# Kernel optimization log

Measured on AMD Instinct MI355X. Metric: run time of the kernel, lower is better.

## Reference

```python
import jax, jax.numpy as jnp
import numpy as np

GROUPS = 32
EPS = 1e-5
NUM_HEADS = 8
HEAD_DIM = 64
CHANNELS = 512


def group_norm(x, scale, bias):
    # x: [b, h, w, c]; normalize over (h, w, channels-within-group)
    b, h, w, c = x.shape
    xg = x.reshape(b, h, w, GROUPS, c // GROUPS)
    mean = jnp.mean(xg, axis=(1, 2, 4), keepdims=True)
    var = jnp.var(xg, axis=(1, 2, 4), keepdims=True)
    xg = (xg - mean) * jax.lax.rsqrt(var + EPS)
    return xg.reshape(b, h, w, c) * scale + bias


def setup_inputs() -> dict:
    key = jax.random.key(0)
    ks = jax.random.split(key, 8)
    b, hs, ws, c = 8, 32, 32, CHANNELS
    inner = NUM_HEADS * HEAD_DIM
    return {
        "x": jax.random.normal(ks[0], (b, hs, ws, c), dtype=jnp.float32),
        "t": jax.random.normal(ks[1], (b,), dtype=jnp.float32),
        "gn_scale": jnp.ones((c,), dtype=jnp.float32),
        "gn_bias": jnp.zeros((c,), dtype=jnp.float32),
        "w_qkv": jax.random.normal(ks[2], (c, 3 * inner), dtype=jnp.float32) * 0.02,
        "b_qkv": jnp.zeros((3 * inner,), dtype=jnp.float32),
        "w_out": jax.random.normal(ks[3], (inner, c), dtype=jnp.float32) * 0.02,
        "b_out": jnp.zeros((c,), dtype=jnp.float32),
    }


def reference(x, t, gn_scale, gn_bias, w_qkv, b_qkv, w_out, b_out):
    b, hs, ws, c = x.shape
    # NOTE: original reassigns x = GroupNorm(x); the residual uses the NORMALIZED x.
    xn = group_norm(x, gn_scale, gn_bias)
    x_flat = xn.reshape(b, hs * ws, c)                      # [b, s, c]
    qkv = x_flat @ w_qkv + b_qkv                            # [b, s, 3*nh*hd]
    qkv = qkv.reshape(b, hs * ws, NUM_HEADS, 3 * HEAD_DIM)
    q, k, v = jnp.split(qkv, 3, axis=-1)                    # each [b, s, nh, hd]
    q = q / jnp.sqrt(jnp.float32(HEAD_DIM))
    q = q.transpose(0, 2, 1, 3)                             # [b, nh, s, hd]
    k = k.transpose(0, 2, 1, 3)
    v = v.transpose(0, 2, 1, 3)
    attn = jax.nn.softmax(jnp.einsum('bhqd,bhkd->bhqk', q, k), axis=-1)
    out = jnp.einsum('bhqk,bhkd->bhqd', attn, v)            # [b, nh, s, hd]
    out = out.transpose(0, 2, 1, 3).reshape(b, hs * ws, NUM_HEADS * HEAD_DIM)
    h = out @ w_out + b_out                                 # [b, s, c]
    h = h.reshape(b, hs, ws, c)
    return xn + h
```

## Files before the change

### kernel.cpp

```cpp
#include <hip/hip_runtime.h>
#include <hip/hip_bf16.h>


#define B_    8
#define S_    1024
#define C_    512
#define NH    8
#define HD    64
#define QKVC  1536
#define GROUPS 32
#define GSIZE  16
#define EPSV   1e-5f
#define QSCL  0.18033688f

using frag8 = __attribute__((ext_vector_type(8))) short;
using f32x4 = __attribute__((ext_vector_type(4))) float;

__device__ __forceinline__ float bf2f(unsigned short u) {
    union { unsigned int i; float f; } v; v.i = ((unsigned int)u) << 16; return v.f;
}
__device__ __forceinline__ unsigned short f2bf(float f) {
    union { float f; unsigned int i; } v; v.f = f;
    unsigned int x = v.i;
    return (unsigned short)((x + 0x7fffu + ((x >> 16) & 1u)) >> 16);
}
__device__ __forceinline__ unsigned int pk2bf(float a, float b) {
    union { float f; unsigned int u; } x, y; x.f = a; y.f = b;
    return __builtin_amdgcn_perm(y.u + 0x8000u, x.u + 0x8000u, 0x07060302u);
}
__device__ __forceinline__ float fexp2(float x) {
#if __has_builtin(__builtin_amdgcn_exp2f)
    return __builtin_amdgcn_exp2f(x);
#else
    return exp2f(x);
#endif
}
__device__ __forceinline__ f32x4 zero4() {
    f32x4 z; z[0] = 0.f; z[1] = 0.f; z[2] = 0.f; z[3] = 0.f; return z;
}
__device__ __forceinline__ void gl_lds(const unsigned short* gp, unsigned short* lp) {
    __builtin_amdgcn_global_load_lds(
        (const __attribute__((address_space(1))) void*)gp,
        (__attribute__((address_space(3))) void*)lp, 16, 0, 0);
}

__global__ __launch_bounds__(256) void prep_kernel(
        const float* __restrict__ w_qkv, const float* __restrict__ w_out,
        unsigned short* __restrict__ wqkvT, unsigned short* __restrict__ woutT,
        const float* __restrict__ x,
        const float* __restrict__ scale, const float* __restrict__ bias,
        unsigned short* __restrict__ xn) {
    __shared__ unsigned short xcache[16384];
    __shared__ float s_red[8];
    int id = blockIdx.x;
    int t = threadIdx.x;
    if (id < 1024) {
        float* tile = (float*)xcache;
        const float* in; unsigned short* out; int N, n0, k0;
        if (id < 768) { in = w_qkv; out = wqkvT; N = QKVC; n0 = (id % 48) * 32; k0 = (id / 48) * 32; }
        else { int i2 = id - 768; in = w_out; out = woutT; N = C_; n0 = (i2 % 16) * 32; k0 = (i2 / 16) * 32; }
        for (int i = 0; i < 4; ++i) {
            int idx = t + i * 256; int r = idx >> 5, c = idx & 31;
            tile[r * 33 + c] = in[(size_t)(k0 + r) * N + n0 + c];
        }
        __syncthreads();
        for (int i = 0; i < 4; ++i) {
            int idx = t + i * 256; int r = idx >> 5, c = idx & 31;
            out[(size_t)(n0 + r) * C_ + k0 + c] = f2bf(tile[c * 33 + r]);
        }
        return;
    }
    int bg = id - 1024;
    int b = bg >> 5, g = bg & 31;
    const float* xb = x + (size_t)b * S_ * C_;

    float sum = 0.f, ss = 0.f;
    for (int i = 0; i < 16; ++i) {
        int idx = t + i * 256;
        int row = idx >> 2, j = idx & 3;
        float4 v = *(const float4*)(xb + (size_t)row * C_ + g * GSIZE + j * 4);
        sum += v.x + v.y + v.z + v.w;
        ss  += v.x * v.x + v.y * v.y + v.z * v.z + v.w * v.w;
        uint2 c;
        c.x = pk2bf(v.x, v.y);
        c.y = pk2bf(v.z, v.w);
        *(uint2*)(&xcache[idx * 4]) = c;
    }
    for (int off = 1; off < 64; off <<= 1) {
        sum += __shfl_xor(sum, off);
        ss  += __shfl_xor(ss,  off);
    }
    int wid = t >> 6;
    if ((t & 63) == 0) { s_red[wid] = sum; s_red[4 + wid] = ss; }
    __syncthreads();
    sum = s_red[0] + s_red[1] + s_red[2] + s_red[3];
    ss  = s_red[4] + s_red[5] + s_red[6] + s_red[7];
    float mean = sum * (1.f / 16384.f);
    float var  = ss * (1.f / 16384.f) - mean * mean;
    float rinv = rsqrtf(var + EPSV);

    float sc[16], bi[16];
    for (int u = 0; u < 16; ++u) {
        sc[u] = scale[g * GSIZE + u];
        bi[u] = bias[g * GSIZE + u];
    }
    for (int i = 0; i < 16; ++i) {
        int idx = t + i * 256;
        int row = idx >> 2, j = idx & 3;
        uint2 c = *(const uint2*)(&xcache[idx * 4]);
        float v0 = bf2f((unsigned short)(c.x & 0xffffu));
        float v1 = bf2f((unsigned short)(c.x >> 16));
        float v2 = bf2f((unsigned short)(c.y & 0xffffu));
        float v3 = bf2f((unsigned short)(c.y >> 16));
        int c0 = j * 4;
        float f0 = (v0 - mean) * rinv * sc[c0 + 0] + bi[c0 + 0];
        float f1 = (v1 - mean) * rinv * sc[c0 + 1] + bi[c0 + 1];
        float f2 = (v2 - mean) * rinv * sc[c0 + 2] + bi[c0 + 2];
        float f3 = (v3 - mean) * rinv * sc[c0 + 3] + bi[c0 + 3];
        uint2 o;
        o.x = pk2bf(f0, f1);
        o.y = pk2bf(f2, f3);
        *(uint2*)(xn + (size_t)b * S_ * C_ + (size_t)row * C_ + g * GSIZE + c0) = o;
    }
}

template<int MODE>
__global__ __launch_bounds__(256) void gemm_kernel(
        const unsigned short* __restrict__ A,
        const unsigned short* __restrict__ Bt,
        const float* __restrict__ bias,
        const unsigned short* __restrict__ resid,
        unsigned short* __restrict__ outA,
        unsigned short* __restrict__ outV,
        float* __restrict__ outF,
        int M, int N, int K) {
    __shared__ unsigned short As[2][128 * 32];
    __shared__ unsigned short Bs[2][128 * 32];
    int m0 = blockIdx.y * 128, n0 = blockIdx.x * 128;
    int t = threadIdx.x;
    int wid = t >> 6, lane = t & 63;
    int quad = lane >> 4, l16 = lane & 15;
    int wm = (wid >> 1) * 64, wn = (wid & 1) * 64;

    f32x4 acc[4][4];
    for (int mi = 0; mi < 4; ++mi)
        for (int ni = 0; ni < 4; ++ni) acc[mi][ni] = zero4();

    int srow = t >> 2, sseg = t & 3;
    auto stage = [&](int k0, int buf) {
        for (int i = 0; i < 2; ++i) {
            gl_lds(A + (size_t)(m0 + i * 64 + srow) * K + k0 + sseg * 8,
                   &As[buf][(size_t)(i * 256 + wid * 64) * 8]);
            gl_lds(Bt + (size_t)(n0 + i * 64 + srow) * K + k0 + sseg * 8,
                   &Bs[buf][(size_t)(i * 256 + wid * 64) * 8]);
        }
    };

    stage(0, 0);
    int nk = K >> 5;
    for (int i = 0; i < nk; ++i) {
        __syncthreads();
        if (i + 1 < nk) stage((i + 1) << 5, (i + 1) & 1);
        int buf = i & 1;

        frag8 bfrag[4], afrag[4];
        for (int ni = 0; ni < 4; ++ni)
            bfrag[ni] = *(const frag8*)(&Bs[buf][(wn + ni * 16 + l16) * 32 + quad * 8]);
        for (int mi = 0; mi < 4; ++mi)
            afrag[mi] = *(const frag8*)(&As[buf][(wm + mi * 16 + l16) * 32 + quad * 8]);

        for (int mi = 0; mi < 4; ++mi)
            for (int ni = 0; ni < 4; ++ni)
                acc[mi][ni] = __builtin_amdgcn_mfma_f32_16x16x32_bf16(
                    afrag[mi], bfrag[ni], acc[mi][ni], 0, 0, 0);
    }

    for (int ni = 0; ni < 4; ++ni) {
        int c0 = n0 + wn + ni * 16;
        float bv = bias[c0 + l16];
        if (MODE == 0) {
            int h = c0 / 192, rr = c0 % 192;
            if (rr >= 128) {
                int d = rr - 128 + l16;
                int bidx = m0 >> 10;
                unsigned short* vp = outV + (((size_t)bidx * NH + h) * HD + d) * S_
                                   + (m0 & 1023) + wm + quad * 4;
                for (int mi = 0; mi < 4; ++mi) {
                    uint2 pk;
                    pk.x = pk2bf(acc[mi][ni][0] + bv, acc[mi][ni][1] + bv);
                    pk.y = pk2bf(acc[mi][ni][2] + bv, acc[mi][ni][3] + bv);
                    *(uint2*)(vp + mi * 16) = pk;
                }
            } else {
                float scl = (rr < 64) ? QSCL : 1.0f;
                int colk = h * 128 + rr + l16;
                for (int mi = 0; mi < 4; ++mi)
                    for (int r = 0; r < 4; ++r) {
                        int row = m0 + wm + mi * 16 + quad * 4 + r;
                        outA[(size_t)row * 1024 + colk] = f2bf((acc[mi][ni][r] + bv) * scl);
                    }
            }
        } else {
            int col = c0 + l16;
            for (int mi = 0; mi < 4; ++mi)
                for (int r = 0; r < 4; ++r) {
                    int row = m0 + wm + mi * 16 + quad * 4 + r;
                    float v = acc[mi][ni][r] + bv + bf2f(resid[(size_t)row * N + col]);
                    outF[(size_t)row * N + col] = v;
                }
        }
    }
}

__global__ __launch_bounds__(256) void attn_kernel(
        const unsigned short* __restrict__ kq,
        const unsigned short* __restrict__ vT,
        unsigned short* __restrict__ attn_out) {
    int i = blockIdx.x;
    int xcd = i & 7, slot = i >> 3;
    int bh = xcd * 8 + (slot >> 4);
    int qt = slot & 15;
    int b = bh >> 3, h = bh & 7;

    int t = threadIdx.x;
    int wid = t >> 6, lane = t & 63, quad = lane >> 4, l16 = lane & 15;
    int q0 = qt * 64 + wid * 16;

    __shared__ unsigned short Ks[2][2][2048];
    __shared__ unsigned short Vs[2][2][2048];

    const unsigned short* qrow = kq + ((size_t)b * S_ + q0 + l16) * 1024 + h * 128;
    frag8 qf0 = *(const frag8*)(qrow + quad * 8);
    frag8 qf1 = *(const frag8*)(qrow + 32 + quad * 8);

    frag8 ones;
    for (int i2 = 0; i2 < 8; ++i2) ones[i2] = (short)0x3f80;

    f32x4 o[4], ol;
    ol = zero4();
    for (int dt = 0; dt < 4; ++dt) o[dt] = zero4();

    const unsigned short* kbase = kq + (size_t)b * S_ * 1024 + h * 128 + 64;
    const unsigned short* vbase = vT + ((size_t)b * NH + h) * HD * S_;

    int kdh = wid & 1, krh = wid >> 1;
    int krow = krh * 16 + (lane >> 2);
    int kseg = lane & 3;
    int vd = wid * 16 + (lane >> 2);
    int vseg = lane & 3;
    int vkh = vseg >> 1, vsp = vseg & 1;
    int vbase1 = vsp * 16 + vkh * 4;

    auto stageK = [&](int j0, int buf, int half) {
        gl_lds(kbase + (size_t)(j0 + krow) * 1024 + kdh * 32 + kseg * 8,
               &Ks[buf][half][kdh * 1024 + krh * 512]);
    };
    auto loadV = [&](int j0) {
        return *(const uint4*)(vbase + (size_t)vd * S_ + j0 + vseg * 8);
    };
    auto writeV = [&](uint4 w, int buf, int half) {
        unsigned short* vdst = &Vs[buf][half][vd * 32];
        uint2 g1; g1.x = w.x; g1.y = w.y;
        uint2 g2; g2.x = w.z; g2.y = w.w;
        *(uint2*)(vdst + vbase1)     = g1;
        *(uint2*)(vdst + vbase1 + 8) = g2;
    };

    stageK(0, 0, 0);  stageK(32, 0, 1);
    writeV(loadV(0), 0, 0);  writeV(loadV(32), 0, 1);

    for (int it = 0; it < S_ / 64; ++it) {
        int cur = it & 1, nxt = cur ^ 1;
        __syncthreads();
        uint4 vn0, vn1;
        bool more = (it < S_ / 64 - 1);
        if (more) {
            int jn = (it + 1) * 64;
            stageK(jn, nxt, 0);
            stageK(jn + 32, nxt, 1);
            vn0 = loadV(jn);
            vn1 = loadV(jn + 32);
        }

        for (int half = 0; half < 2; ++half) {
            frag8 kf[2][2];
            for (int kh = 0; kh < 2; ++kh)
                for (int dh = 0; dh < 2; ++dh)
                    kf[kh][dh] = *(const frag8*)(&Ks[cur][half][dh * 1024 + (kh * 16 + l16) * 32 + quad * 8]);

            f32x4 s[2];
            for (int kh = 0; kh < 2; ++kh) {
                f32x4 acc = zero4();
                acc = __builtin_amdgcn_mfma_f32_16x16x32_bf16(kf[kh][0], qf0, acc, 0, 0, 0);
                acc = __builtin_amdgcn_mfma_f32_16x16x32_bf16(kf[kh][1], qf1, acc, 0, 0, 0);
                s[kh] = acc;
            }

            union { frag8 f; unsigned int u[4]; } pfu;
            pfu.u[0] = pk2bf(fexp2(s[0][0]), fexp2(s[0][1]));
            pfu.u[1] = pk2bf(fexp2(s[0][2]), fexp2(s[0][3]));
            pfu.u[2] = pk2bf(fexp2(s[1][0]), fexp2(s[1][1]));
            pfu.u[3] = pk2bf(fexp2(s[1][2]), fexp2(s[1][3]));

            frag8 vf[4];
            for (int dt = 0; dt < 4; ++dt)
                vf[dt] = *(const frag8*)(&Vs[cur][half][(dt * 16 + l16) * 32 + quad * 8]);

            ol = __builtin_amdgcn_mfma_f32_16x16x32_bf16(pfu.f, ones, ol, 0, 0, 0);
            for (int dt = 0; dt < 4; ++dt)
                o[dt] = __builtin_amdgcn_mfma_f32_16x16x32_bf16(pfu.f, vf[dt], o[dt], 0, 0, 0);
        }

        if (more) {
            writeV(vn0, nxt, 0);
            writeV(vn1, nxt, 1);
        }
    }

    for (int r = 0; r < 4; ++r) {
        float inv = 1.0f / ol[r];
        int qrw = q0 + quad * 4 + r;
        for (int dt = 0; dt < 4; ++dt) {
            int ch = h * HD + dt * 16 + l16;
            attn_out[((size_t)b * S_ + qrw) * C_ + ch] = f2bf(o[dt][r] * inv);
        }
    }
}

extern "C" void kernel_launch(void* const* d_in, const int* in_sizes, int n_in,
                              void* d_out, int out_size, void* d_ws, size_t ws_size,
                              hipStream_t stream) {
    const float* x        = (const float*)d_in[0];
    const float* gn_scale = (const float*)d_in[2];
    const float* gn_bias  = (const float*)d_in[3];
    const float* w_qkv    = (const float*)d_in[4];
    const float* b_qkv    = (const float*)d_in[5];
    const float* w_out    = (const float*)d_in[6];
    const float* b_out    = (const float*)d_in[7];
    float* out = (float*)d_out;

    char* ws = (char*)d_ws;
    unsigned short* xn    = (unsigned short*)(ws);
    unsigned short* kq    = (unsigned short*)(ws + ((size_t)8  << 20));
    unsigned short* attn  = (unsigned short*)(ws + ((size_t)24 << 20));
    unsigned short* vT    = (unsigned short*)(ws + ((size_t)32 << 20));
    unsigned short* wqkvT = (unsigned short*)(ws + ((size_t)40 << 20));
    unsigned short* woutT = (unsigned short*)(ws + ((size_t)40 << 20) + ((size_t)3 << 19));

    prep_kernel<<<dim3(1280), 256, 0, stream>>>(
        w_qkv, w_out, wqkvT, woutT, x, gn_scale, gn_bias, xn);

    gemm_kernel<0><<<dim3(QKVC / 128, (B_ * S_) / 128), 256, 0, stream>>>(
        xn, wqkvT, b_qkv, nullptr, kq, vT, nullptr, B_ * S_, QKVC, C_);

    attn_kernel<<<dim3(1024), 256, 0, stream>>>(kq, vT, attn);

    gemm_kernel<1><<<dim3(C_ / 128, (B_ * S_) / 128), 256, 0, stream>>>(
        attn, woutT, b_out, xn, nullptr, nullptr, out, B_ * S_, C_, C_);
}
```

Measured before the change: 157.6 us.

## Split GEMMs, remap blocks per XCD, double attention query tile, swizzle LDS

The templated GEMM becomes two specialized kernels. Each uses an XCD-aware block index remap, and the output projection uses 64x128 tiles so 512 blocks fill the GPU. The attention kernel now processes 32 query rows per wave, reusing each K/V LDS fragment for two query groups and halving the grid to 512 blocks. It also XOR-swizzles the K and V LDS layouts to avoid bank conflicts and adds s_setprio around the MFMA groups. More accumulators per wave raise register pressure and may lower occupancy.

After: 152.3 us. -3.4%, faster.

```diff
diff --git a/kernel.cpp b/kernel.cpp
--- a/kernel.cpp
+++ b/kernel.cpp
@@ -124,19 +124,18 @@
     }
 }
 
-template<int MODE>
-__global__ __launch_bounds__(256) void gemm_kernel(
+__global__ __launch_bounds__(256) void gemm_qkv_kernel(
         const unsigned short* __restrict__ A,
         const unsigned short* __restrict__ Bt,
         const float* __restrict__ bias,
-        const unsigned short* __restrict__ resid,
         unsigned short* __restrict__ outA,
-        unsigned short* __restrict__ outV,
-        float* __restrict__ outF,
-        int M, int N, int K) {
+        unsigned short* __restrict__ outV) {
     __shared__ unsigned short As[2][128 * 32];
     __shared__ unsigned short Bs[2][128 * 32];
-    int m0 = blockIdx.y * 128, n0 = blockIdx.x * 128;
+    unsigned int flat = blockIdx.y * 12u + blockIdx.x;
+    unsigned int nid = (flat & 7u) * 96u + (flat >> 3);
+    int my = nid / 12u, mx = nid % 12u;
+    int m0 = my * 128, n0 = mx * 128;
     int t = threadIdx.x;
     int wid = t >> 6, lane = t & 63;
     int quad = lane >> 4, l16 = lane & 15;
@@ -149,15 +148,15 @@
     int srow = t >> 2, sseg = t & 3;
     auto stage = [&](int k0, int buf) {
         for (int i = 0; i < 2; ++i) {
-            gl_lds(A + (size_t)(m0 + i * 64 + srow) * K + k0 + sseg * 8,
+            gl_lds(A + (size_t)(m0 + i * 64 + srow) * C_ + k0 + sseg * 8,
                    &As[buf][(size_t)(i * 256 + wid * 64) * 8]);
-            gl_lds(Bt + (size_t)(n0 + i * 64 + srow) * K + k0 + sseg * 8,
+            gl_lds(Bt + (size_t)(n0 + i * 64 + srow) * C_ + k0 + sseg * 8,
                    &Bs[buf][(size_t)(i * 256 + wid * 64) * 8]);
         }
     };
 
     stage(0, 0);
-    int nk = K >> 5;
+    const int nk = C_ >> 5;
     for (int i = 0; i < nk; ++i) {
         __syncthreads();
         if (i + 1 < nk) stage((i + 1) << 5, (i + 1) & 1);
@@ -178,37 +177,88 @@
     for (int ni = 0; ni < 4; ++ni) {
         int c0 = n0 + wn + ni * 16;
         float bv = bias[c0 + l16];
-        if (MODE == 0) {
-            int h = c0 / 192, rr = c0 % 192;
-            if (rr >= 128) {
-                int d = rr - 128 + l16;
-                int bidx = m0 >> 10;
-                unsigned short* vp = outV + (((size_t)bidx * NH + h) * HD + d) * S_
-                                   + (m0 & 1023) + wm + quad * 4;
-                for (int mi = 0; mi < 4; ++mi) {
-                    uint2 pk;
-                    pk.x = pk2bf(acc[mi][ni][0] + bv, acc[mi][ni][1] + bv);
-                    pk.y = pk2bf(acc[mi][ni][2] + bv, acc[mi][ni][3] + bv);
-                    *(uint2*)(vp + mi * 16) = pk;
-                }
-            } else {
-                float scl = (rr < 64) ? QSCL : 1.0f;
-                int colk = h * 128 + rr + l16;
-                for (int mi = 0; mi < 4; ++mi)
-                    for (int r = 0; r < 4; ++r) {
-                        int row = m0 + wm + mi * 16 + quad * 4 + r;
-                        outA[(size_t)row * 1024 + colk] = f2bf((acc[mi][ni][r] + bv) * scl);
-                    }
+        int h = c0 / 192, rr = c0 % 192;
+        if (rr >= 128) {
+            int d = rr - 128 + l16;
+            int bidx = m0 >> 10;
+            unsigned short* vp = outV + (((size_t)bidx * NH + h) * HD + d) * S_
+                               + (m0 & 1023) + wm + quad * 4;
+            for (int mi = 0; mi < 4; ++mi) {
+                uint2 pk;
+                pk.x = pk2bf(acc[mi][ni][0] + bv, acc[mi][ni][1] + bv);
+                pk.y = pk2bf(acc[mi][ni][2] + bv, acc[mi][ni][3] + bv);
+                *(uint2*)(vp + mi * 16) = pk;
             }
         } else {
-            int col = c0 + l16;
+            float scl = (rr < 64) ? QSCL : 1.0f;
+            int colk = h * 128 + rr + l16;
             for (int mi = 0; mi < 4; ++mi)
                 for (int r = 0; r < 4; ++r) {
                     int row = m0 + wm + mi * 16 + quad * 4 + r;
-                    float v = acc[mi][ni][r] + bv + bf2f(resid[(size_t)row * N + col]);
-                    outF[(size_t)row * N + col] = v;
+                    outA[(size_t)row * 1024 + colk] = f2bf((acc[mi][ni][r] + bv) * scl);
                 }
         }
+    }
+}
+
+__global__ __launch_bounds__(256) void gemm_out_kernel(
+        const unsigned short* __restrict__ A,
+        const unsigned short* __restrict__ Bt,
+        const float* __restrict__ bias,
+        const unsigned short* __restrict__ resid,
+        float* __restrict__ outF) {
+    __shared__ unsigned short As[2][64 * 32];
+    __shared__ unsigned short Bs[2][128 * 32];
+    unsigned int flat = blockIdx.x;
+    unsigned int nid = (flat & 7u) * 64u + (flat >> 3);
+    int my = nid >> 2, mx = nid & 3;
+    int m0 = my * 64, n0 = mx * 128;
+    int t = threadIdx.x;
+    int wid = t >> 6, lane = t & 63;
+    int quad = lane >> 4, l16 = lane & 15;
+    int wm = (wid >> 1) * 32, wn = (wid & 1) * 64;
+
+    f32x4 acc[2][4];
+    for (int mi = 0; mi < 2; ++mi)
+        for (int ni = 0; ni < 4; ++ni) acc[mi][ni] = zero4();
+
+    int srow = t >> 2, sseg = t & 3;
+    auto stage = [&](int k0, int buf) {
+        gl_lds(A + (size_t)(m0 + srow) * C_ + k0 + sseg * 8,
+               &As[buf][(size_t)wid * 512]);
+        for (int i = 0; i < 2; ++i)
+            gl_lds(Bt + (size_t)(n0 + i * 64 + srow) * C_ + k0 + sseg * 8,
+                   &Bs[buf][(size_t)(i * 256 + wid * 64) * 8]);
+    };
+
+    stage(0, 0);
+    const int nk = C_ >> 5;
+    for (int i = 0; i < nk; ++i) {
+        __syncthreads();
+        if (i + 1 < nk) stage((i + 1) << 5, (i + 1) & 1);
+        int buf = i & 1;
+
+        frag8 bfrag[4], afrag[2];
+        for (int ni = 0; ni < 4; ++ni)
+            bfrag[ni] = *(const frag8*)(&Bs[buf][(wn + ni * 16 + l16) * 32 + quad * 8]);
+        for (int mi = 0; mi < 2; ++mi)
+            afrag[mi] = *(const frag8*)(&As[buf][(wm + mi * 16 + l16) * 32 + quad * 8]);
+
+        for (int mi = 0; mi < 2; ++mi)
+            for (int ni = 0; ni < 4; ++ni)
+                acc[mi][ni] = __builtin_amdgcn_mfma_f32_16x16x32_bf16(
+                    afrag[mi], bfrag[ni], acc[mi][ni], 0, 0, 0);
+    }
+
+    for (int ni = 0; ni < 4; ++ni) {
+        int col = n0 + wn + ni * 16 + l16;
+        float bv = bias[col];
+        for (int mi = 0; mi < 2; ++mi)
+            for (int r = 0; r < 4; ++r) {
+                int row = m0 + wm + mi * 16 + quad * 4 + r;
+                float v = acc[mi][ni][r] + bv + bf2f(resid[(size_t)row * C_ + col]);
+                outF[(size_t)row * C_ + col] = v;
+            }
     }
 }
 
@@ -218,38 +268,48 @@
         unsigned short* __restrict__ attn_out) {
     int i = blockIdx.x;
     int xcd = i & 7, slot = i >> 3;
-    int bh = xcd * 8 + (slot >> 4);
-    int qt = slot & 15;
+    int bh = xcd * 8 + (slot >> 3);
+    int qt = slot & 7;
     int b = bh >> 3, h = bh & 7;
 
     int t = threadIdx.x;
     int wid = t >> 6, lane = t & 63, quad = lane >> 4, l16 = lane & 15;
-    int q0 = qt * 64 + wid * 16;
+    int q0 = qt * 128 + wid * 32;
 
     __shared__ unsigned short Ks[2][2][2048];
     __shared__ unsigned short Vs[2][2][2048];
 
-    const unsigned short* qrow = kq + ((size_t)b * S_ + q0 + l16) * 1024 + h * 128;
-    frag8 qf0 = *(const frag8*)(qrow + quad * 8);
-    frag8 qf1 = *(const frag8*)(qrow + 32 + quad * 8);
+    const unsigned short* qrow0 = kq + ((size_t)b * S_ + q0 + l16) * 1024 + h * 128;
+    const unsigned short* qrow1 = qrow0 + (size_t)16 * 1024;
+    frag8 qf[2][2];
+    qf[0][0] = *(const frag8*)(qrow0 + quad * 8);
+    qf[0][1] = *(const frag8*)(qrow0 + 32 + quad * 8);
+    qf[1][0] = *(const frag8*)(qrow1 + quad * 8);
+    qf[1][1] = *(const frag8*)(qrow1 + 32 + quad * 8);
 
     frag8 ones;
     for (int i2 = 0; i2 < 8; ++i2) ones[i2] = (short)0x3f80;
 
-    f32x4 o[4], ol;
-    ol = zero4();
-    for (int dt = 0; dt < 4; ++dt) o[dt] = zero4();
+    f32x4 o[2][4], ol[2];
+    for (int g = 0; g < 2; ++g) {
+        ol[g] = zero4();
+        for (int dt = 0; dt < 4; ++dt) o[g][dt] = zero4();
+    }
 
     const unsigned short* kbase = kq + (size_t)b * S_ * 1024 + h * 128 + 64;
     const unsigned short* vbase = vT + ((size_t)b * NH + h) * HD * S_;
 
     int kdh = wid & 1, krh = wid >> 1;
     int krow = krh * 16 + (lane >> 2);
-    int kseg = lane & 3;
+    int kseg = (lane & 3) ^ ((lane >> 3) & 3);
     int vd = wid * 16 + (lane >> 2);
     int vseg = lane & 3;
     int vkh = vseg >> 1, vsp = vseg & 1;
-    int vbase1 = vsp * 16 + vkh * 4;
+    int vsw = (lane >> 3) & 3;
+    int vo1 = (((vsp * 2) ^ vsw) * 8) + vkh * 4;
+    int vo2 = (((vsp * 2 + 1) ^ vsw) * 8) + vkh * 4;
+
+    int ksw = (l16 >> 1) & 3;
 
     auto stageK = [&](int j0, int buf, int half) {
         gl_lds(kbase + (size_t)(j0 + krow) * 1024 + kdh * 32 + kseg * 8,
@@ -262,8 +322,8 @@
         unsigned short* vdst = &Vs[buf][half][vd * 32];
         uint2 g1; g1.x = w.x; g1.y = w.y;
         uint2 g2; g2.x = w.z; g2.y = w.w;
-        *(uint2*)(vdst + vbase1)     = g1;
-        *(uint2*)(vdst + vbase1 + 8) = g2;
+        *(uint2*)(vdst + vo1) = g1;
+        *(uint2*)(vdst + vo2) = g2;
     };
 
     stageK(0, 0, 0);  stageK(32, 0, 1);
@@ -286,29 +346,35 @@
             frag8 kf[2][2];
             for (int kh = 0; kh < 2; ++kh)
                 for (int dh = 0; dh < 2; ++dh)
-                    kf[kh][dh] = *(const frag8*)(&Ks[cur][half][dh * 1024 + (kh * 16 + l16) * 32 + quad * 8]);
-
-            f32x4 s[2];
-            for (int kh = 0; kh < 2; ++kh) {
-                f32x4 acc = zero4();
-                acc = __builtin_amdgcn_mfma_f32_16x16x32_bf16(kf[kh][0], qf0, acc, 0, 0, 0);
-                acc = __builtin_amdgcn_mfma_f32_16x16x32_bf16(kf[kh][1], qf1, acc, 0, 0, 0);
-                s[kh] = acc;
-            }
-
-            union { frag8 f; unsigned int u[4]; } pfu;
-            pfu.u[0] = pk2bf(fexp2(s[0][0]), fexp2(s[0][1]));
-            pfu.u[1] = pk2bf(fexp2(s[0][2]), fexp2(s[0][3]));
-            pfu.u[2] = pk2bf(fexp2(s[1][0]), fexp2(s[1][1]));
-            pfu.u[3] = pk2bf(fexp2(s[1][2]), fexp2(s[1][3]));
+                    kf[kh][dh] = *(const frag8*)(&Ks[cur][half][dh * 1024
+                        + (kh * 16 + l16) * 32 + ((quad ^ ksw) * 8)]);
 
             frag8 vf[4];
             for (int dt = 0; dt < 4; ++dt)
-                vf[dt] = *(const frag8*)(&Vs[cur][half][(dt * 16 + l16) * 32 + quad * 8]);
-
-            ol = __builtin_amdgcn_mfma_f32_16x16x32_bf16(pfu.f, ones, ol, 0, 0, 0);
-            for (int dt = 0; dt < 4; ++dt)
-                o[dt] = __builtin_amdgcn_mfma_f32_16x16x32_bf16(pfu.f, vf[dt], o[dt], 0, 0, 0);
+                vf[dt] = *(const frag8*)(&Vs[cur][half][(dt * 16 + l16) * 32
+                        + ((quad ^ ksw) * 8)]);
+
+            for (int g = 0; g < 2; ++g) {
+                f32x4 s0 = zero4(), s1 = zero4();
+                __builtin_amdgcn_s_setprio(1);
+                s0 = __builtin_amdgcn_mfma_f32_16x16x32_bf16(kf[0][0], qf[g][0], s0, 0, 0, 0);
+                s0 = __builtin_amdgcn_mfma_f32_16x16x32_bf16(kf[0][1], qf[g][1], s0, 0, 0, 0);
+                s1 = __builtin_amdgcn_mfma_f32_16x16x32_bf16(kf[1][0], qf[g][0], s1, 0, 0, 0);
+                s1 = __builtin_amdgcn_mfma_f32_16x16x32_bf16(kf[1][1], qf[g][1], s1, 0, 0, 0);
+                __builtin_amdgcn_s_setprio(0);
+
+                union { frag8 f; unsigned int u[4]; } pfu;
+                pfu.u[0] = pk2bf(fexp2(s0[0]), fexp2(s0[1]));
+                pfu.u[1] = pk2bf(fexp2(s0[2]), fexp2(s0[3]));
+                pfu.u[2] = pk2bf(fexp2(s1[0]), fexp2(s1[1]));
+                pfu.u[3] = pk2bf(fexp2(s1[2]), fexp2(s1[3]));
+
+                __builtin_amdgcn_s_setprio(1);
+                ol[g] = __builtin_amdgcn_mfma_f32_16x16x32_bf16(pfu.f, ones, ol[g], 0, 0, 0);
+                for (int dt = 0; dt < 4; ++dt)
+                    o[g][dt] = __builtin_amdgcn_mfma_f32_16x16x32_bf16(pfu.f, vf[dt], o[g][dt], 0, 0, 0);
+                __builtin_amdgcn_s_setprio(0);
+            }
         }
 
         if (more) {
@@ -317,14 +383,15 @@
         }
     }
 
-    for (int r = 0; r < 4; ++r) {
-        float inv = 1.0f / ol[r];
-        int qrw = q0 + quad * 4 + r;
-        for (int dt = 0; dt < 4; ++dt) {
-            int ch = h * HD + dt * 16 + l16;
-            attn_out[((size_t)b * S_ + qrw) * C_ + ch] = f2bf(o[dt][r] * inv);
-        }
-    }
+    for (int g = 0; g < 2; ++g)
+        for (int r = 0; r < 4; ++r) {
+            float inv = 1.0f / ol[g][r];
+            int qrw = q0 + g * 16 + quad * 4 + r;
+            for (int dt = 0; dt < 4; ++dt) {
+                int ch = h * HD + dt * 16 + l16;
+                attn_out[((size_t)b * S_ + qrw) * C_ + ch] = f2bf(o[g][dt][r] * inv);
+            }
+        }
 }
 
 extern "C" void kernel_launch(void* const* d_in, const int* in_sizes, int n_in,
@@ -350,11 +417,11 @@
     prep_kernel<<<dim3(1280), 256, 0, stream>>>(
         w_qkv, w_out, wqkvT, woutT, x, gn_scale, gn_bias, xn);
 
-    gemm_kernel<0><<<dim3(QKVC / 128, (B_ * S_) / 128), 256, 0, stream>>>(
-        xn, wqkvT, b_qkv, nullptr, kq, vT, nullptr, B_ * S_, QKVC, C_);
-
-    attn_kernel<<<dim3(1024), 256, 0, stream>>>(kq, vT, attn);
-
-    gemm_kernel<1><<<dim3(C_ / 128, (B_ * S_) / 128), 256, 0, stream>>>(
-        attn, woutT, b_out, xn, nullptr, nullptr, out, B_ * S_, C_, C_);
-}
+    gemm_qkv_kernel<<<dim3(QKVC / 128, (B_ * S_) / 128), 256, 0, stream>>>(
+        xn, wqkvT, b_qkv, kq, vT);
+
+    attn_kernel<<<dim3(512), 256, 0, stream>>>(kq, vT, attn);
+
+    gemm_out_kernel<<<dim3(512), 256, 0, stream>>>(
+        attn, woutT, b_out, xn, out);
+}
```
